# Kernel tuning notes

Measured on AMD Instinct MI355X. Metric: run time of the kernel, lower is better.

Reference implementation:

```python
import jax, jax.numpy as jnp
import numpy as np

EMBED_DIM = 1024
NUM_HEADS = 16
HEAD_DIM = EMBED_DIM // NUM_HEADS


def setup_inputs() -> dict:
    key = jax.random.key(0)
    ks = jax.random.split(key, 9)
    B, S, D = 4, 2048, EMBED_DIM
    s = 1.0 / np.sqrt(D)
    inp = {
        "x": jax.random.normal(ks[0], (B, S, D), dtype=jnp.float32),
        "Wq": jax.random.uniform(ks[1], (D, D), jnp.float32, -s, s),
        "bq": jax.random.uniform(ks[2], (D,), jnp.float32, -s, s),
        "Wk": jax.random.uniform(ks[3], (D, D), jnp.float32, -s, s),
        "bk": jax.random.uniform(ks[4], (D,), jnp.float32, -s, s),
        "Wv": jax.random.uniform(ks[5], (D, D), jnp.float32, -s, s),
        "bv": jax.random.uniform(ks[6], (D,), jnp.float32, -s, s),
        "Wo": jax.random.uniform(ks[7], (D, D), jnp.float32, -s, s),
        "bo": jax.random.uniform(ks[8], (D,), jnp.float32, -s, s),
    }
    return inp


def reference(x, Wq, bq, Wk, bk, Wv, bv, Wo, bo):
    B, S, D = x.shape
    H, Hd = NUM_HEADS, HEAD_DIM
    scale = 1.0 / jnp.sqrt(jnp.asarray(Hd, x.dtype))

    def split_heads(t):  # (B,S,D) -> (B,H,S,Hd)
        return t.reshape(B, S, H, Hd).transpose(0, 2, 1, 3)

    q = split_heads(x @ Wq + bq)
    k = split_heads(x @ Wk + bk)
    v = split_heads(x @ Wv + bv)

    scores = jnp.einsum("bhqd,bhkd->bhqk", q, k) * scale
    attn = jax.nn.softmax(scores, axis=-1)  # dropout is identity in eval mode
    out = jnp.einsum("bhqk,bhkd->bhqd", attn, v)
    out = out.transpose(0, 2, 1, 3).reshape(B, S, D)
    return out @ Wo + bo
```

## Files before the change

kernel.cpp:

```cpp
#include <hip/hip_runtime.h>
#include <cstdint>

typedef unsigned short u16;
typedef uint32_t u32;
typedef float f32x4 __attribute__((ext_vector_type(4)));
typedef short s16x8 __attribute__((ext_vector_type(8)));
typedef u16 u16x4 __attribute__((ext_vector_type(4)));
typedef u32 u32x2 __attribute__((ext_vector_type(2)));
typedef u32 u32x4 __attribute__((ext_vector_type(4)));

__device__ __forceinline__ u16 f2bf(float f) {
  u32 u = __builtin_bit_cast(u32, f);
  u += 0x7FFFu + ((u >> 16) & 1u);
  return (u16)(u >> 16);
}

__device__ __forceinline__ u32 pack2bf_trunc(float lo, float hi) {
  return __builtin_amdgcn_perm(__builtin_bit_cast(u32, hi),
                               __builtin_bit_cast(u32, lo), 0x07060302u);
}

template <typename T>
__device__ __forceinline__ T ldv(const void* p) {
  T v;
  __builtin_memcpy(&v, __builtin_assume_aligned(p, 16), sizeof(T));
  return v;
}

__device__ __forceinline__ void gload_lds16(const void* g, void* l) {
  __builtin_amdgcn_global_load_lds((const __attribute__((address_space(1))) void*)g,
                                   (__attribute__((address_space(3))) void*)l, 16, 0, 0);
}

__global__ __launch_bounds__(256) void cvt_x_k(const float* __restrict__ in,
                                               u16* __restrict__ out) {
  const int i = (blockIdx.x * 256 + threadIdx.x) * 4;
  float4 v = *(const float4*)(in + i);
  u16x4 o;
  o.x = f2bf(v.x); o.y = f2bf(v.y); o.z = f2bf(v.z); o.w = f2bf(v.w);
  *(u16x4*)(out + i) = o;
}

__global__ __launch_bounds__(256) void prep_w_k(const float* __restrict__ Wq,
                                                const float* __restrict__ Wk,
                                                const float* __restrict__ Wv,
                                                const float* __restrict__ Wo,
                                                u16* __restrict__ out) {
  __shared__ u16 t[64][72];
  const float* W = (blockIdx.z == 0) ? Wq : (blockIdx.z == 1) ? Wk
                  : (blockIdx.z == 2) ? Wv : Wo;
  u16* O = out + (size_t)blockIdx.z * 1024 * 1024;
  const int n0 = blockIdx.x * 64, k0 = blockIdx.y * 64;
  const int tid = threadIdx.x;
#pragma unroll
  for (int i = 0; i < 16; ++i) {
    int e = i * 256 + tid;
    int r = e >> 6, c = e & 63;
    t[r][c] = f2bf(W[(size_t)(k0 + r) * 1024 + n0 + c]);
  }
  __syncthreads();
#pragma unroll
  for (int i = 0; i < 16; ++i) {
    int e = i * 256 + tid;
    int rr = e >> 6, cc = e & 63;
    O[(size_t)(n0 + rr) * 1024 + k0 + cc] = t[cc][rr];
  }
}

__global__ __launch_bounds__(512, 2) void gemm_qkv_k(const u16* __restrict__ A,
                                                     const u16* __restrict__ Wt,
                                                     const float* __restrict__ bq,
                                                     const float* __restrict__ bk,
                                                     const float* __restrict__ bv,
                                                     u16* __restrict__ Qh,
                                                     u16* __restrict__ Kh,
                                                     u16* __restrict__ Vt,
                                                     float qscale) {
  constexpr int K = 1024;
  __shared__ __attribute__((aligned(16))) u16 As[3][256][64];
  __shared__ __attribute__((aligned(16))) u16 Bs[3][128][64];
  const int tid = threadIdx.x;
  const int l = tid & 63, w = tid >> 6;
  const int lr = l & 15, lg = l >> 4;
  const int m0 = blockIdx.x * 256;
  const int ng = blockIdx.y * 128;
  const int seg = ng >> 10;
  const int n0 = ng & 1023;
  const u16* Bt = Wt + ((size_t)seg << 20);
  const int wr = (w >> 1) * 64, wc = (w & 1) * 64;
  const int rT = tid >> 3;
  const int cSw = (((tid & 7) ^ (rT & 7)) << 3);

  f32x4 acc[4][4] = {};

#define GSTAGE(buf, kt)                                                         \
  do {                                                                          \
    _Pragma("unroll")                                                           \
    for (int i = 0; i < 4; ++i)                                                 \
      gload_lds16(A + (size_t)(m0 + i * 64 + rT) * K + (kt) + cSw,              \
                  &As[buf][i * 64][0] + (size_t)w * 512);                       \
    _Pragma("unroll")                                                           \
    for (int i = 0; i < 2; ++i)                                                 \
      gload_lds16(Bt + (size_t)(n0 + i * 64 + rT) * K + (kt) + cSw,             \
                  &Bs[buf][i * 64][0] + (size_t)w * 512);                       \
  } while (0)

  GSTAGE(0, 0);
  GSTAGE(1, 64);
  asm volatile("s_waitcnt vmcnt(6)" ::: "memory");
  __builtin_amdgcn_s_barrier();

  int bcur = 0, bst = 2;
  for (int t = 0; t < 16; ++t) {
    if (t < 14) {
      GSTAGE(bst, (t + 2) * 64);
      asm volatile("s_waitcnt vmcnt(12)" ::: "memory");
    } else if (t == 14) {
      asm volatile("s_waitcnt vmcnt(6)" ::: "memory");
    } else {
      asm volatile("s_waitcnt vmcnt(0)" ::: "memory");
    }
    __builtin_amdgcn_s_barrier();
#pragma unroll
    for (int kk = 0; kk < 2; ++kk) {
      s16x8 a[4], b[4];
#pragma unroll
      for (int mi = 0; mi < 4; ++mi)
        a[mi] = ldv<s16x8>(&As[bcur][wr + mi * 16 + lr][((kk * 4 + lg) ^ (lr & 7)) << 3]);
#pragma unroll
      for (int ni = 0; ni < 4; ++ni)
        b[ni] = ldv<s16x8>(&Bs[bcur][wc + ni * 16 + lr][((kk * 4 + lg) ^ (lr & 7)) << 3]);
#pragma unroll
      for (int mi = 0; mi < 4; ++mi)
#pragma unroll
        for (int ni = 0; ni < 4; ++ni)
          acc[mi][ni] = __builtin_amdgcn_mfma_f32_16x16x32_bf16(a[mi], b[ni], acc[mi][ni], 0, 0, 0);
    }
    __builtin_amdgcn_s_barrier();
    bcur = (bcur == 2) ? 0 : bcur + 1;
    bst = (bst == 2) ? 0 : bst + 1;
  }
#undef GSTAGE

  const float* bias = (seg == 0) ? bq : (seg == 1) ? bk : bv;
  const float scale = (seg == 0) ? qscale : 1.0f;
  u16* outp = (seg == 0) ? Qh : (seg == 1) ? Kh : Vt;

  u16* Cb = &As[0][0][0];
  const int bb = m0 >> 11;
  const int sbase = m0 & 2047;

#pragma unroll
  for (int p = 0; p < 2; ++p) {
    __syncthreads();
    if ((wc >> 6) == p) {
#pragma unroll
      for (int ni = 0; ni < 4; ++ni) {
        const int c = ni * 16 + lr;
        const float bvv = bias[n0 + p * 64 + c];
#pragma unroll
        for (int mi = 0; mi < 4; ++mi) {
#pragma unroll
          for (int r = 0; r < 4; ++r) {
            const int row = wr + mi * 16 + lg * 4 + r;
            Cb[row * 64 + ((((c >> 3) ^ (row & 7)) << 3) | (c & 7))] =
                f2bf((acc[mi][ni][r] + bvv) * scale);
          }
        }
      }
    }
    __syncthreads();
    const int h = (n0 + p * 64) >> 6;
    if (seg <= 1) {
      const int row = tid >> 1;
      const int s = sbase + row;
#pragma unroll
      for (int j = 0; j < 4; ++j) {
        const int c = (tid & 1) * 32 + j * 8;
        s16x8 v = ldv<s16x8>(&Cb[row * 64 + (((c >> 3) ^ (row & 7)) << 3)]);
        const int chunk = (seg == 0) ? (c >> 3) : (((c >> 3) ^ (s & 7)) & 7);
        *(s16x8*)(outp + ((size_t)((bb << 4) + h) * 2048 + s) * 64 + (chunk << 3)) = v;
      }
    } else {
      const int hd = tid & 63;
#pragma unroll
      for (int j = 0; j < 4; ++j) {
        const int s0 = (tid >> 6) * 32 + j * 8;
        u16 vals[8];
#pragma unroll
        for (int i = 0; i < 8; ++i) {
          const int row = s0 + i;
          vals[i] = Cb[row * 64 + ((((hd >> 3) ^ (row & 7)) << 3) | (hd & 7))];
        }
        const int sl = sbase + s0;
        const int swz = (((sl >> 3) & 7) ^ (hd & 7)) & 7;
        *(s16x8*)(outp + ((size_t)((bb << 4) + h) * 64 + hd) * 2048 +
                  ((sl & ~63) | (swz << 3))) = *(s16x8*)vals;
      }
    }
  }
}

__global__ __launch_bounds__(512, 2) void gemm_o_k(const u16* __restrict__ A,
                                                   const u16* __restrict__ Bt,
                                                   const float* __restrict__ bias,
                                                   float* __restrict__ outp) {
  constexpr int K = 1024;
  __shared__ __attribute__((aligned(16))) u16 As[3][256][64];
  __shared__ __attribute__((aligned(16))) u16 Bs[3][128][64];
  const int tid = threadIdx.x;
  const int l = tid & 63, w = tid >> 6;
  const int lr = l & 15, lg = l >> 4;
  const int m0 = blockIdx.x * 256, n0 = blockIdx.y * 128;
  const int wr = (w >> 1) * 64, wc = (w & 1) * 64;
  const int rT = tid >> 3;
  const int cSw = (((tid & 7) ^ (rT & 7)) << 3);

  f32x4 acc[4][4] = {};

#define GSTAGE(buf, kt)                                                         \
  do {                                                                          \
    _Pragma("unroll")                                                           \
    for (int i = 0; i < 4; ++i)                                                 \
      gload_lds16(A + (size_t)(m0 + i * 64 + rT) * K + (kt) + cSw,              \
                  &As[buf][i * 64][0] + (size_t)w * 512);                       \
    _Pragma("unroll")                                                           \
    for (int i = 0; i < 2; ++i)                                                 \
      gload_lds16(Bt + (size_t)(n0 + i * 64 + rT) * K + (kt) + cSw,             \
                  &Bs[buf][i * 64][0] + (size_t)w * 512);                       \
  } while (0)

  GSTAGE(0, 0);
  GSTAGE(1, 64);
  asm volatile("s_waitcnt vmcnt(6)" ::: "memory");
  __builtin_amdgcn_s_barrier();

  int bcur = 0, bst = 2;
  for (int t = 0; t < 16; ++t) {
    if (t < 14) {
      GSTAGE(bst, (t + 2) * 64);
      asm volatile("s_waitcnt vmcnt(12)" ::: "memory");
    } else if (t == 14) {
      asm volatile("s_waitcnt vmcnt(6)" ::: "memory");
    } else {
      asm volatile("s_waitcnt vmcnt(0)" ::: "memory");
    }
    __builtin_amdgcn_s_barrier();
#pragma unroll
    for (int kk = 0; kk < 2; ++kk) {
      s16x8 a[4], b[4];
#pragma unroll
      for (int mi = 0; mi < 4; ++mi)
        a[mi] = ldv<s16x8>(&As[bcur][wr + mi * 16 + lr][((kk * 4 + lg) ^ (lr & 7)) << 3]);
#pragma unroll
      for (int ni = 0; ni < 4; ++ni)
        b[ni] = ldv<s16x8>(&Bs[bcur][wc + ni * 16 + lr][((kk * 4 + lg) ^ (lr & 7)) << 3]);
#pragma unroll
      for (int mi = 0; mi < 4; ++mi)
#pragma unroll
        for (int ni = 0; ni < 4; ++ni)
          acc[mi][ni] = __builtin_amdgcn_mfma_f32_16x16x32_bf16(a[mi], b[ni], acc[mi][ni], 0, 0, 0);
    }
    __builtin_amdgcn_s_barrier();
    bcur = (bcur == 2) ? 0 : bcur + 1;
    bst = (bst == 2) ? 0 : bst + 1;
  }
#undef GSTAGE

#pragma unroll
  for (int ni = 0; ni < 4; ++ni) {
    const int col = n0 + wc + ni * 16 + lr;
    const float bv = bias[col];
#pragma unroll
    for (int mi = 0; mi < 4; ++mi)
#pragma unroll
      for (int r = 0; r < 4; ++r) {
        const int rowm = m0 + wr + mi * 16 + lg * 4 + r;
        outp[(size_t)rowm * 1024 + col] = acc[mi][ni][r] + bv;
      }
  }
}

__global__ __launch_bounds__(256, 2) void attn_k(const u16* __restrict__ Qh,
                                                 const u16* __restrict__ Kg,
                                                 const u16* __restrict__ Vg,
                                                 u16* __restrict__ Oattn) {
  __shared__ __attribute__((aligned(16))) u16 Kbuf[2][4096];
  __shared__ __attribute__((aligned(16))) u16 Vbuf[2][4096];
  __shared__ __attribute__((aligned(16))) u16 P_lds[4][16][64];
  const int tid = threadIdx.x, l = tid & 63, w = tid >> 6;
  const int lr = l & 15, lg = l >> 4;
  const int bh = blockIdx.y;
  const int q0 = blockIdx.x * 256 + w * 64;
  const u16* Q = Qh + (size_t)bh * (2048 * 64);
  const u16* K = Kg + (size_t)bh * (2048 * 64);
  const u16* V = Vg + (size_t)bh * (64 * 2048);

  s16x8 qf[4][2];
#pragma unroll
  for (int f = 0; f < 4; ++f)
#pragma unroll
    for (int kk = 0; kk < 2; ++kk)
      qf[f][kk] = ldv<s16x8>(Q + (size_t)(q0 + f * 16 + lr) * 64 + kk * 32 + lg * 8);

  const u32 one2 = 0x3F803F80u;
  const s16x8 onesv = __builtin_bit_cast(s16x8, (u32x4){one2, one2, one2, one2});

  f32x4 acc[4][4] = {};
  f32x4 lsum[4] = {};

#define STAGE(buf, kv0)                                                                 \
  do {                                                                                  \
    gload_lds16(K + (size_t)(kv0) * 64 + (size_t)tid * 8, &Kbuf[buf][w * 512]);         \
    gload_lds16(K + (size_t)(kv0) * 64 + 2048 + (size_t)tid * 8,                        \
                &Kbuf[buf][2048 + w * 512]);                                            \
    gload_lds16(V + (size_t)(tid >> 3) * 2048 + (kv0) + (tid & 7) * 8,                  \
                &Vbuf[buf][w * 512]);                                                   \
    gload_lds16(V + (size_t)((tid >> 3) + 32) * 2048 + (kv0) + (tid & 7) * 8,           \
                &Vbuf[buf][2048 + w * 512]);                                            \
  } while (0)

  STAGE(0, 0);

  for (int t = 0; t < 32; ++t) {
    const int cur = t & 1;
    if (t < 31) {
      STAGE(cur ^ 1, (t + 1) * 64);
      asm volatile("s_waitcnt vmcnt(4)" ::: "memory");
    } else {
      asm volatile("s_waitcnt vmcnt(0)" ::: "memory");
    }
    __builtin_amdgcn_s_barrier();

    s16x8 pf[4][2];
#pragma unroll
    for (int kvc = 0; kvc < 2; ++kvc) {
      f32x4 s2[4][2] = {};
      __builtin_amdgcn_s_setprio(1);
#pragma unroll
      for (int t2 = 0; t2 < 2; ++t2) {
        const int tt = kvc * 2 + t2;
        s16x8 k0 = ldv<s16x8>(&Kbuf[cur][(tt * 16 + lr) * 64 + ((lg ^ (lr & 7)) << 3)]);
        s16x8 k1 = ldv<s16x8>(&Kbuf[cur][(tt * 16 + lr) * 64 + (((4 + lg) ^ (lr & 7)) << 3)]);
#pragma unroll
        for (int f = 0; f < 4; ++f) {
          s2[f][t2] = __builtin_amdgcn_mfma_f32_16x16x32_bf16(k0, qf[f][0], s2[f][t2], 0, 0, 0);
          s2[f][t2] = __builtin_amdgcn_mfma_f32_16x16x32_bf16(k1, qf[f][1], s2[f][t2], 0, 0, 0);
        }
      }
      __builtin_amdgcn_s_setprio(0);

#pragma unroll
      for (int f = 0; f < 4; ++f) {
#pragma unroll
        for (int t2 = 0; t2 < 2; ++t2)
#pragma unroll
          for (int r = 0; r < 4; ++r)
            s2[f][t2][r] = __builtin_amdgcn_exp2f(s2[f][t2][r]);
#pragma unroll
        for (int t2 = 0; t2 < 2; ++t2) {
          const int tt = kvc * 2 + t2;
          u32x2 pw;
          pw.x = pack2bf_trunc(s2[f][t2][0], s2[f][t2][1]);
          pw.y = pack2bf_trunc(s2[f][t2][2], s2[f][t2][3]);
          const int off = (((tt * 2 + (lg >> 1)) ^ (lr & 7)) << 3) + ((lg & 1) << 2);
          *(u32x2*)&P_lds[w][lr][off] = pw;
        }
        pf[f][kvc] = ldv<s16x8>(&P_lds[w][lr][((kvc * 4 + lg) ^ (lr & 7)) << 3]);
        lsum[f] = __builtin_amdgcn_mfma_f32_16x16x32_bf16(pf[f][kvc], onesv, lsum[f], 0, 0, 0);
      }
    }

    __builtin_amdgcn_s_setprio(1);
#pragma unroll
    for (int dt = 0; dt < 4; ++dt) {
      s16x8 v0 = ldv<s16x8>(&Vbuf[cur][(dt * 16 + lr) * 64 + ((lg ^ (lr & 7)) << 3)]);
      s16x8 v1 = ldv<s16x8>(&Vbuf[cur][(dt * 16 + lr) * 64 + (((4 + lg) ^ (lr & 7)) << 3)]);
#pragma unroll
      for (int f = 0; f < 4; ++f) {
        acc[f][dt] = __builtin_amdgcn_mfma_f32_16x16x32_bf16(pf[f][0], v0, acc[f][dt], 0, 0, 0);
        acc[f][dt] = __builtin_amdgcn_mfma_f32_16x16x32_bf16(pf[f][1], v1, acc[f][dt], 0, 0, 0);
      }
    }
    __builtin_amdgcn_s_setprio(0);
    __builtin_amdgcn_s_barrier();
  }
#undef STAGE

  const int b = bh >> 4, h = bh & 15;
#pragma unroll
  for (int f = 0; f < 4; ++f) {
    float li[4];
#pragma unroll
    for (int r = 0; r < 4; ++r) li[r] = __builtin_amdgcn_rcpf(lsum[f][r]);
#pragma unroll
    for (int dt = 0; dt < 4; ++dt)
#pragma unroll
      for (int r = 0; r < 4; ++r) {
        const int q = q0 + f * 16 + lg * 4 + r;
        Oattn[(size_t)((b << 11) + q) * 1024 + (h << 6) + dt * 16 + lr] =
            f2bf(acc[f][dt][r] * li[r]);
      }
  }
}

extern "C" void kernel_launch(void* const* d_in, const int* in_sizes, int n_in,
                              void* d_out, int out_size, void* d_ws, size_t ws_size,
                              hipStream_t stream) {
  const float* x  = (const float*)d_in[0];
  const float* Wq = (const float*)d_in[1];
  const float* bq = (const float*)d_in[2];
  const float* Wk = (const float*)d_in[3];
  const float* bk = (const float*)d_in[4];
  const float* Wv = (const float*)d_in[5];
  const float* bv = (const float*)d_in[6];
  const float* Wo = (const float*)d_in[7];
  const float* bo = (const float*)d_in[8];

  char* ws = (char*)d_ws;
  const size_t MB = 1u << 20;
  u16* xb = (u16*)(ws);
  u16* wt = (u16*)(ws + 16 * MB);
  u16* Qh = (u16*)(ws + 24 * MB);
  u16* Kh = (u16*)(ws + 40 * MB);
  u16* Vt = (u16*)(ws + 56 * MB);
  u16* attn = xb;

  const float qscale = 0.125f * 1.44269504088896f;

  cvt_x_k<<<dim3(8192), dim3(256), 0, stream>>>(x, xb);
  prep_w_k<<<dim3(16, 16, 4), dim3(256), 0, stream>>>(Wq, Wk, Wv, Wo, wt);
  gemm_qkv_k<<<dim3(32, 24), dim3(512), 0, stream>>>(xb, wt, bq, bk, bv, Qh, Kh, Vt, qscale);
  attn_k<<<dim3(8, 64), dim3(256), 0, stream>>>(Qh, Kh, Vt, attn);
  gemm_o_k<<<dim3(32, 8), dim3(512), 0, stream>>>(attn, wt + 3 * 1048576, bo, (float*)d_out);
}
```

Baseline: 201.7 us.

## Merge QKV and output GEMMs into one templated 256x256-tile kernel

Replaces the 256x128-tile GEMMs with one templated 256x256-tile kernel. It has 8 waves each computing 128x64, double buffering instead of triple, and occupancy 1. Larger tiles raise arithmetic intensity and reuse of the loaded A and B tiles. In exchange the output GEMM launches only 128 blocks, under half the CUs, and the QKV GEMM 384, so CU utilization and latency hiding may drop.

Result: slower. 227.3 us (+12.7%).

```diff
diff --git a/kernel.cpp b/kernel.cpp
--- a/kernel.cpp
+++ b/kernel.cpp
@@ -67,31 +67,34 @@
   }
 }
 
-__global__ __launch_bounds__(512, 2) void gemm_qkv_k(const u16* __restrict__ A,
-                                                     const u16* __restrict__ Wt,
-                                                     const float* __restrict__ bq,
-                                                     const float* __restrict__ bk,
-                                                     const float* __restrict__ bv,
-                                                     u16* __restrict__ Qh,
-                                                     u16* __restrict__ Kh,
-                                                     u16* __restrict__ Vt,
-                                                     float qscale) {
+template <int OMODE>
+__global__ __launch_bounds__(512, 1) void gemm256_k(const u16* __restrict__ A,
+                                                    const u16* __restrict__ Wt,
+                                                    const float* __restrict__ bq,
+                                                    const float* __restrict__ bk,
+                                                    const float* __restrict__ bv,
+                                                    u16* __restrict__ Qh,
+                                                    u16* __restrict__ Kh,
+                                                    u16* __restrict__ Vt,
+                                                    float* __restrict__ Oo,
+                                                    float qscale) {
   constexpr int K = 1024;
-  __shared__ __attribute__((aligned(16))) u16 As[3][256][64];
-  __shared__ __attribute__((aligned(16))) u16 Bs[3][128][64];
+  __shared__ __attribute__((aligned(16))) u16 As[2][256][64];
+  __shared__ __attribute__((aligned(16))) u16 Bs[2][256][64];
   const int tid = threadIdx.x;
   const int l = tid & 63, w = tid >> 6;
   const int lr = l & 15, lg = l >> 4;
+  const int wm = w >> 2, wn = w & 3;
   const int m0 = blockIdx.x * 256;
-  const int ng = blockIdx.y * 128;
-  const int seg = ng >> 10;
-  const int n0 = ng & 1023;
+  int seg, n0;
+  if constexpr (OMODE == 0) { seg = blockIdx.y >> 2; n0 = (blockIdx.y & 3) * 256; }
+  else { seg = 3; n0 = blockIdx.y * 256; }
   const u16* Bt = Wt + ((size_t)seg << 20);
-  const int wr = (w >> 1) * 64, wc = (w & 1) * 64;
   const int rT = tid >> 3;
   const int cSw = (((tid & 7) ^ (rT & 7)) << 3);
-
-  f32x4 acc[4][4] = {};
+  const int xk = lr & 7;
+
+  f32x4 acc[8][4] = {};
 
 #define GSTAGE(buf, kt)                                                         \
   do {                                                                          \
@@ -100,184 +103,111 @@
       gload_lds16(A + (size_t)(m0 + i * 64 + rT) * K + (kt) + cSw,              \
                   &As[buf][i * 64][0] + (size_t)w * 512);                       \
     _Pragma("unroll")                                                           \
-    for (int i = 0; i < 2; ++i)                                                 \
+    for (int i = 0; i < 4; ++i)                                                 \
       gload_lds16(Bt + (size_t)(n0 + i * 64 + rT) * K + (kt) + cSw,             \
                   &Bs[buf][i * 64][0] + (size_t)w * 512);                       \
   } while (0)
 
   GSTAGE(0, 0);
-  GSTAGE(1, 64);
-  asm volatile("s_waitcnt vmcnt(6)" ::: "memory");
+  asm volatile("s_waitcnt vmcnt(0)" ::: "memory");
   __builtin_amdgcn_s_barrier();
 
-  int bcur = 0, bst = 2;
   for (int t = 0; t < 16; ++t) {
-    if (t < 14) {
-      GSTAGE(bst, (t + 2) * 64);
-      asm volatile("s_waitcnt vmcnt(12)" ::: "memory");
-    } else if (t == 14) {
-      asm volatile("s_waitcnt vmcnt(6)" ::: "memory");
+    const int cur = t & 1;
+    if (t < 15) {
+      GSTAGE(cur ^ 1, (t + 1) * 64);
+      asm volatile("s_waitcnt vmcnt(8)" ::: "memory");
     } else {
       asm volatile("s_waitcnt vmcnt(0)" ::: "memory");
     }
     __builtin_amdgcn_s_barrier();
 #pragma unroll
     for (int kk = 0; kk < 2; ++kk) {
-      s16x8 a[4], b[4];
-#pragma unroll
-      for (int mi = 0; mi < 4; ++mi)
-        a[mi] = ldv<s16x8>(&As[bcur][wr + mi * 16 + lr][((kk * 4 + lg) ^ (lr & 7)) << 3]);
+      s16x8 b[4];
 #pragma unroll
       for (int ni = 0; ni < 4; ++ni)
-        b[ni] = ldv<s16x8>(&Bs[bcur][wc + ni * 16 + lr][((kk * 4 + lg) ^ (lr & 7)) << 3]);
-#pragma unroll
-      for (int mi = 0; mi < 4; ++mi)
+        b[ni] = ldv<s16x8>(&Bs[cur][wn * 64 + ni * 16 + lr][((kk * 4 + lg) ^ xk) << 3]);
+#pragma unroll
+      for (int mi = 0; mi < 8; ++mi) {
+        s16x8 a = ldv<s16x8>(&As[cur][wm * 128 + mi * 16 + lr][((kk * 4 + lg) ^ xk) << 3]);
 #pragma unroll
         for (int ni = 0; ni < 4; ++ni)
-          acc[mi][ni] = __builtin_amdgcn_mfma_f32_16x16x32_bf16(a[mi], b[ni], acc[mi][ni], 0, 0, 0);
+          acc[mi][ni] = __builtin_amdgcn_mfma_f32_16x16x32_bf16(a, b[ni], acc[mi][ni], 0, 0, 0);
+      }
     }
     __builtin_amdgcn_s_barrier();
-    bcur = (bcur == 2) ? 0 : bcur + 1;
-    bst = (bst == 2) ? 0 : bst + 1;
   }
 #undef GSTAGE
 
-  const float* bias = (seg == 0) ? bq : (seg == 1) ? bk : bv;
-  const float scale = (seg == 0) ? qscale : 1.0f;
-  u16* outp = (seg == 0) ? Qh : (seg == 1) ? Kh : Vt;
-
-  u16* Cb = &As[0][0][0];
-  const int bb = m0 >> 11;
-  const int sbase = m0 & 2047;
-
-#pragma unroll
-  for (int p = 0; p < 2; ++p) {
-    __syncthreads();
-    if ((wc >> 6) == p) {
-#pragma unroll
-      for (int ni = 0; ni < 4; ++ni) {
-        const int c = ni * 16 + lr;
-        const float bvv = bias[n0 + p * 64 + c];
-#pragma unroll
-        for (int mi = 0; mi < 4; ++mi) {
-#pragma unroll
-          for (int r = 0; r < 4; ++r) {
-            const int row = wr + mi * 16 + lg * 4 + r;
-            Cb[row * 64 + ((((c >> 3) ^ (row & 7)) << 3) | (c & 7))] =
-                f2bf((acc[mi][ni][r] + bvv) * scale);
+  if constexpr (OMODE == 1) {
+#pragma unroll
+    for (int ni = 0; ni < 4; ++ni) {
+      const int col = n0 + wn * 64 + ni * 16 + lr;
+      const float bvv = bq[col];
+#pragma unroll
+      for (int mi = 0; mi < 8; ++mi)
+#pragma unroll
+        for (int r = 0; r < 4; ++r) {
+          const int row = m0 + wm * 128 + mi * 16 + lg * 4 + r;
+          Oo[(size_t)row * 1024 + col] = acc[mi][ni][r] + bvv;
+        }
+    }
+    return;
+  } else {
+    const float* bias = (seg == 0) ? bq : (seg == 1) ? bk : bv;
+    const float scale = (seg == 0) ? qscale : 1.0f;
+    u16* outp = (seg == 0) ? Qh : (seg == 1) ? Kh : Vt;
+    u16* Cb = &As[0][0][0];
+    const int bb = m0 >> 11;
+    const int sbase = m0 & 2047;
+#pragma unroll
+    for (int p = 0; p < 4; ++p) {
+      __syncthreads();
+      if (wn == p) {
+#pragma unroll
+        for (int ni = 0; ni < 4; ++ni) {
+          const int c = ni * 16 + lr;
+          const float bvv = bias[n0 + p * 64 + c];
+#pragma unroll
+          for (int mi = 0; mi < 8; ++mi)
+#pragma unroll
+            for (int r = 0; r < 4; ++r) {
+              const int row = wm * 128 + mi * 16 + lg * 4 + r;
+              Cb[row * 64 + ((((c >> 3) ^ (row & 7)) << 3) | (c & 7))] =
+                  f2bf((acc[mi][ni][r] + bvv) * scale);
+            }
+        }
+      }
+      __syncthreads();
+      const int h = (n0 + p * 64) >> 6;
+      if (seg <= 1) {
+        const int row = tid >> 1;
+        const int s = sbase + row;
+#pragma unroll
+        for (int j = 0; j < 4; ++j) {
+          const int c = (tid & 1) * 32 + j * 8;
+          s16x8 v = ldv<s16x8>(&Cb[row * 64 + (((c >> 3) ^ (row & 7)) << 3)]);
+          const int chunk = (seg == 0) ? (c >> 3) : (((c >> 3) ^ (s & 7)) & 7);
+          *(s16x8*)(outp + ((size_t)((bb << 4) + h) * 2048 + s) * 64 + (chunk << 3)) = v;
+        }
+      } else {
+        const int hd = tid & 63;
+#pragma unroll
+        for (int j = 0; j < 4; ++j) {
+          const int s0 = (tid >> 6) * 32 + j * 8;
+          u16 vals[8];
+#pragma unroll
+          for (int i = 0; i < 8; ++i) {
+            const int row = s0 + i;
+            vals[i] = Cb[row * 64 + ((((hd >> 3) ^ (row & 7)) << 3) | (hd & 7))];
           }
-        }
-      }
-    }
-    __syncthreads();
-    const int h = (n0 + p * 64) >> 6;
-    if (seg <= 1) {
-      const int row = tid >> 1;
-      const int s = sbase + row;
-#pragma unroll
-      for (int j = 0; j < 4; ++j) {
-        const int c = (tid & 1) * 32 + j * 8;
-        s16x8 v = ldv<s16x8>(&Cb[row * 64 + (((c >> 3) ^ (row & 7)) << 3)]);
-        const int chunk = (seg == 0) ? (c >> 3) : (((c >> 3) ^ (s & 7)) & 7);
-        *(s16x8*)(outp + ((size_t)((bb << 4) + h) * 2048 + s) * 64 + (chunk << 3)) = v;
-      }
-    } else {
-      const int hd = tid & 63;
-#pragma unroll
-      for (int j = 0; j < 4; ++j) {
-        const int s0 = (tid >> 6) * 32 + j * 8;
-        u16 vals[8];
-#pragma unroll
-        for (int i = 0; i < 8; ++i) {
-          const int row = s0 + i;
-          vals[i] = Cb[row * 64 + ((((hd >> 3) ^ (row & 7)) << 3) | (hd & 7))];
-        }
-        const int sl = sbase + s0;
-        const int swz = (((sl >> 3) & 7) ^ (hd & 7)) & 7;
-        *(s16x8*)(outp + ((size_t)((bb << 4) + h) * 64 + hd) * 2048 +
-                  ((sl & ~63) | (swz << 3))) = *(s16x8*)vals;
-      }
-    }
-  }
-}
-
-__global__ __launch_bounds__(512, 2) void gemm_o_k(const u16* __restrict__ A,
-                                                   const u16* __restrict__ Bt,
-                                                   const float* __restrict__ bias,
-                                                   float* __restrict__ outp) {
-  constexpr int K = 1024;
-  __shared__ __attribute__((aligned(16))) u16 As[3][256][64];
-  __shared__ __attribute__((aligned(16))) u16 Bs[3][128][64];
-  const int tid = threadIdx.x;
-  const int l = tid & 63, w = tid >> 6;
-  const int lr = l & 15, lg = l >> 4;
-  const int m0 = blockIdx.x * 256, n0 = blockIdx.y * 128;
-  const int wr = (w >> 1) * 64, wc = (w & 1) * 64;
-  const int rT = tid >> 3;
-  const int cSw = (((tid & 7) ^ (rT & 7)) << 3);
-
-  f32x4 acc[4][4] = {};
-
-#define GSTAGE(buf, kt)                                                         \
-  do {                                                                          \
-    _Pragma("unroll")                                                           \
-    for (int i = 0; i < 4; ++i)                                                 \
-      gload_lds16(A + (size_t)(m0 + i * 64 + rT) * K + (kt) + cSw,              \
-                  &As[buf][i * 64][0] + (size_t)w * 512);                       \
-    _Pragma("unroll")                                                           \
-    for (int i = 0; i < 2; ++i)                                                 \
-      gload_lds16(Bt + (size_t)(n0 + i * 64 + rT) * K + (kt) + cSw,             \
-                  &Bs[buf][i * 64][0] + (size_t)w * 512);                       \
-  } while (0)
-
-  GSTAGE(0, 0);
-  GSTAGE(1, 64);
-  asm volatile("s_waitcnt vmcnt(6)" ::: "memory");
-  __builtin_amdgcn_s_barrier();
-
-  int bcur = 0, bst = 2;
-  for (int t = 0; t < 16; ++t) {
-    if (t < 14) {
-      GSTAGE(bst, (t + 2) * 64);
-      asm volatile("s_waitcnt vmcnt(12)" ::: "memory");
-    } else if (t == 14) {
-      asm volatile("s_waitcnt vmcnt(6)" ::: "memory");
-    } else {
-      asm volatile("s_waitcnt vmcnt(0)" ::: "memory");
-    }
-    __builtin_amdgcn_s_barrier();
-#pragma unroll
-    for (int kk = 0; kk < 2; ++kk) {
-      s16x8 a[4], b[4];
-#pragma unroll
-      for (int mi = 0; mi < 4; ++mi)
-        a[mi] = ldv<s16x8>(&As[bcur][wr + mi * 16 + lr][((kk * 4 + lg) ^ (lr & 7)) << 3]);
-#pragma unroll
-      for (int ni = 0; ni < 4; ++ni)
-        b[ni] = ldv<s16x8>(&Bs[bcur][wc + ni * 16 + lr][((kk * 4 + lg) ^ (lr & 7)) << 3]);
-#pragma unroll
-      for (int mi = 0; mi < 4; ++mi)
-#pragma unroll
-        for (int ni = 0; ni < 4; ++ni)
-          acc[mi][ni] = __builtin_amdgcn_mfma_f32_16x16x32_bf16(a[mi], b[ni], acc[mi][ni], 0, 0, 0);
-    }
-    __builtin_amdgcn_s_barrier();
-    bcur = (bcur == 2) ? 0 : bcur + 1;
-    bst = (bst == 2) ? 0 : bst + 1;
-  }
-#undef GSTAGE
-
-#pragma unroll
-  for (int ni = 0; ni < 4; ++ni) {
-    const int col = n0 + wc + ni * 16 + lr;
-    const float bv = bias[col];
-#pragma unroll
-    for (int mi = 0; mi < 4; ++mi)
-#pragma unroll
-      for (int r = 0; r < 4; ++r) {
-        const int rowm = m0 + wr + mi * 16 + lg * 4 + r;
-        outp[(size_t)rowm * 1024 + col] = acc[mi][ni][r] + bv;
-      }
+          const int sl = sbase + s0;
+          const int swz = (((sl >> 3) & 7) ^ (hd & 7)) & 7;
+          *(s16x8*)(outp + ((size_t)((bb << 4) + h) * 64 + hd) * 2048 +
+                    ((sl & ~63) | (swz << 3))) = *(s16x8*)vals;
+        }
+      }
+    }
   }
 }
 
@@ -430,7 +360,10 @@
 
   cvt_x_k<<<dim3(8192), dim3(256), 0, stream>>>(x, xb);
   prep_w_k<<<dim3(16, 16, 4), dim3(256), 0, stream>>>(Wq, Wk, Wv, Wo, wt);
-  gemm_qkv_k<<<dim3(32, 24), dim3(512), 0, stream>>>(xb, wt, bq, bk, bv, Qh, Kh, Vt, qscale);
+  gemm256_k<0><<<dim3(32, 12), dim3(512), 0, stream>>>(xb, wt, bq, bk, bv, Qh, Kh, Vt,
+                                                       nullptr, qscale);
   attn_k<<<dim3(8, 64), dim3(256), 0, stream>>>(Qh, Kh, Vt, attn);
-  gemm_o_k<<<dim3(32, 8), dim3(512), 0, stream>>>(attn, wt + 3 * 1048576, bo, (float*)d_out);
-}
+  gemm256_k<1><<<dim3(32, 4), dim3(512), 0, stream>>>(attn, wt, bo, nullptr, nullptr,
+                                                      nullptr, nullptr, nullptr,
+                                                      (float*)d_out, 1.0f);
+}
```

## Enlarge QKV GEMM tile to 256x384 and double attention block to 8 waves

Applied to the files above, without the earlier changes.

The QKV GEMM moves from a 256x128 tile with a triple-buffered pipeline to a 256x384 tile with double buffering. Each wave now holds an 8x6 MFMA accumulator tile, and the epilogue writes scalar bf16 directly to global memory instead of going through LDS and vector stores. The attention kernel now uses 512 threads with 8 waves sharing each K/V tile load, which halves the per-thread staging work. The intent is more operand reuse and fewer K/V loads, at the cost of higher register pressure, lower occupancy (launch bounds 1), a shallower prefetch pipeline, and uncoalesced scalar stores in the GEMM epilogue.

New measurement: 208.9 us. 3.6% more time.

```diff
diff --git a/kernel.cpp b/kernel.cpp
--- a/kernel.cpp
+++ b/kernel.cpp
@@ -67,7 +67,7 @@
   }
 }
 
-__global__ __launch_bounds__(512, 2) void gemm_qkv_k(const u16* __restrict__ A,
+__global__ __launch_bounds__(512, 1) void gemm_qkv_k(const u16* __restrict__ A,
                                                      const u16* __restrict__ Wt,
                                                      const float* __restrict__ bq,
                                                      const float* __restrict__ bk,
@@ -77,21 +77,19 @@
                                                      u16* __restrict__ Vt,
                                                      float qscale) {
   constexpr int K = 1024;
-  __shared__ __attribute__((aligned(16))) u16 As[3][256][64];
-  __shared__ __attribute__((aligned(16))) u16 Bs[3][128][64];
+  __shared__ __attribute__((aligned(16))) u16 As[2][256][64];
+  __shared__ __attribute__((aligned(16))) u16 Bs[2][384][64];
   const int tid = threadIdx.x;
   const int l = tid & 63, w = tid >> 6;
   const int lr = l & 15, lg = l >> 4;
+  const int wm = w >> 2, wn = w & 3;
   const int m0 = blockIdx.x * 256;
-  const int ng = blockIdx.y * 128;
-  const int seg = ng >> 10;
-  const int n0 = ng & 1023;
-  const u16* Bt = Wt + ((size_t)seg << 20);
-  const int wr = (w >> 1) * 64, wc = (w & 1) * 64;
+  const int by = blockIdx.y;
   const int rT = tid >> 3;
   const int cSw = (((tid & 7) ^ (rT & 7)) << 3);
-
-  f32x4 acc[4][4] = {};
+  const int xk = lr & 7;
+
+  f32x4 acc[8][6] = {};
 
 #define GSTAGE(buf, kt)                                                         \
   do {                                                                          \
@@ -100,102 +98,70 @@
       gload_lds16(A + (size_t)(m0 + i * 64 + rT) * K + (kt) + cSw,              \
                   &As[buf][i * 64][0] + (size_t)w * 512);                       \
     _Pragma("unroll")                                                           \
-    for (int i = 0; i < 2; ++i)                                                 \
-      gload_lds16(Bt + (size_t)(n0 + i * 64 + rT) * K + (kt) + cSw,             \
+    for (int i = 0; i < 6; ++i)                                                 \
+      gload_lds16(Wt + (size_t)(by * 384 + i * 64 + rT) * K + (kt) + cSw,       \
                   &Bs[buf][i * 64][0] + (size_t)w * 512);                       \
   } while (0)
 
   GSTAGE(0, 0);
-  GSTAGE(1, 64);
-  asm volatile("s_waitcnt vmcnt(6)" ::: "memory");
+  asm volatile("s_waitcnt vmcnt(0)" ::: "memory");
   __builtin_amdgcn_s_barrier();
 
-  int bcur = 0, bst = 2;
   for (int t = 0; t < 16; ++t) {
-    if (t < 14) {
-      GSTAGE(bst, (t + 2) * 64);
-      asm volatile("s_waitcnt vmcnt(12)" ::: "memory");
-    } else if (t == 14) {
-      asm volatile("s_waitcnt vmcnt(6)" ::: "memory");
+    const int cur = t & 1;
+    if (t < 15) {
+      GSTAGE(cur ^ 1, (t + 1) * 64);
+      asm volatile("s_waitcnt vmcnt(10)" ::: "memory");
     } else {
       asm volatile("s_waitcnt vmcnt(0)" ::: "memory");
     }
     __builtin_amdgcn_s_barrier();
 #pragma unroll
     for (int kk = 0; kk < 2; ++kk) {
-      s16x8 a[4], b[4];
-#pragma unroll
-      for (int mi = 0; mi < 4; ++mi)
-        a[mi] = ldv<s16x8>(&As[bcur][wr + mi * 16 + lr][((kk * 4 + lg) ^ (lr & 7)) << 3]);
-#pragma unroll
-      for (int ni = 0; ni < 4; ++ni)
-        b[ni] = ldv<s16x8>(&Bs[bcur][wc + ni * 16 + lr][((kk * 4 + lg) ^ (lr & 7)) << 3]);
-#pragma unroll
-      for (int mi = 0; mi < 4; ++mi)
-#pragma unroll
-        for (int ni = 0; ni < 4; ++ni)
-          acc[mi][ni] = __builtin_amdgcn_mfma_f32_16x16x32_bf16(a[mi], b[ni], acc[mi][ni], 0, 0, 0);
-    }
-    __builtin_amdgcn_s_barrier();
-    bcur = (bcur == 2) ? 0 : bcur + 1;
-    bst = (bst == 2) ? 0 : bst + 1;
+      s16x8 b[6];
+#pragma unroll
+      for (int ni = 0; ni < 6; ++ni)
+        b[ni] = ldv<s16x8>(&Bs[cur][wn * 96 + ni * 16 + lr][((kk * 4 + lg) ^ xk) << 3]);
+#pragma unroll
+      for (int mi = 0; mi < 8; ++mi) {
+        s16x8 a = ldv<s16x8>(&As[cur][wm * 128 + mi * 16 + lr][((kk * 4 + lg) ^ xk) << 3]);
+#pragma unroll
+        for (int ni = 0; ni < 6; ++ni)
+          acc[mi][ni] = __builtin_amdgcn_mfma_f32_16x16x32_bf16(a, b[ni], acc[mi][ni], 0, 0, 0);
+      }
+    }
+    __builtin_amdgcn_s_barrier();
   }
 #undef GSTAGE
 
-  const float* bias = (seg == 0) ? bq : (seg == 1) ? bk : bv;
-  const float scale = (seg == 0) ? qscale : 1.0f;
-  u16* outp = (seg == 0) ? Qh : (seg == 1) ? Kh : Vt;
-
-  u16* Cb = &As[0][0][0];
-  const int bb = m0 >> 11;
-  const int sbase = m0 & 2047;
-
-#pragma unroll
-  for (int p = 0; p < 2; ++p) {
-    __syncthreads();
-    if ((wc >> 6) == p) {
-#pragma unroll
-      for (int ni = 0; ni < 4; ++ni) {
-        const int c = ni * 16 + lr;
-        const float bvv = bias[n0 + p * 64 + c];
-#pragma unroll
-        for (int mi = 0; mi < 4; ++mi) {
-#pragma unroll
-          for (int r = 0; r < 4; ++r) {
-            const int row = wr + mi * 16 + lg * 4 + r;
-            Cb[row * 64 + ((((c >> 3) ^ (row & 7)) << 3) | (c & 7))] =
-                f2bf((acc[mi][ni][r] + bvv) * scale);
-          }
+  const int gcbase = by * 384 + wn * 96;
+#pragma unroll
+  for (int ni = 0; ni < 6; ++ni) {
+    const int gc0 = gcbase + ni * 16;
+    const int seg = gc0 >> 10;
+    const int col = (gc0 & 1023) + lr;
+    const float* bias = (seg == 0) ? bq : (seg == 1) ? bk : bv;
+    u16* outp = (seg == 0) ? Qh : (seg == 1) ? Kh : Vt;
+    const float scale = (seg == 0) ? qscale : 1.0f;
+    const float bvv = bias[col];
+    const int h = col >> 6, hd = col & 63;
+#pragma unroll
+    for (int mi = 0; mi < 8; ++mi) {
+#pragma unroll
+      for (int r = 0; r < 4; ++r) {
+        const int row = m0 + wm * 128 + mi * 16 + lg * 4 + r;
+        const float v = (acc[mi][ni][r] + bvv) * scale;
+        const int bb = row >> 11, s = row & 2047;
+        const u16 o = f2bf(v);
+        if (seg == 0) {
+          outp[((size_t)((bb << 4) + h) * 2048 + s) * 64 + hd] = o;
+        } else if (seg == 1) {
+          const int hd_swz = ((((hd >> 3) ^ (s & 7)) & 7) << 3) | (hd & 7);
+          outp[((size_t)((bb << 4) + h) * 2048 + s) * 64 + hd_swz] = o;
+        } else {
+          const int s_swz = (s & ~63) | (((((s >> 3) & 7) ^ (hd & 7)) & 7) << 3) | (s & 7);
+          outp[((size_t)((bb << 4) + h) * 64 + hd) * 2048 + s_swz] = o;
         }
-      }
-    }
-    __syncthreads();
-    const int h = (n0 + p * 64) >> 6;
-    if (seg <= 1) {
-      const int row = tid >> 1;
-      const int s = sbase + row;
-#pragma unroll
-      for (int j = 0; j < 4; ++j) {
-        const int c = (tid & 1) * 32 + j * 8;
-        s16x8 v = ldv<s16x8>(&Cb[row * 64 + (((c >> 3) ^ (row & 7)) << 3)]);
-        const int chunk = (seg == 0) ? (c >> 3) : (((c >> 3) ^ (s & 7)) & 7);
-        *(s16x8*)(outp + ((size_t)((bb << 4) + h) * 2048 + s) * 64 + (chunk << 3)) = v;
-      }
-    } else {
-      const int hd = tid & 63;
-#pragma unroll
-      for (int j = 0; j < 4; ++j) {
-        const int s0 = (tid >> 6) * 32 + j * 8;
-        u16 vals[8];
-#pragma unroll
-        for (int i = 0; i < 8; ++i) {
-          const int row = s0 + i;
-          vals[i] = Cb[row * 64 + ((((hd >> 3) ^ (row & 7)) << 3) | (hd & 7))];
-        }
-        const int sl = sbase + s0;
-        const int swz = (((sl >> 3) & 7) ^ (hd & 7)) & 7;
-        *(s16x8*)(outp + ((size_t)((bb << 4) + h) * 64 + hd) * 2048 +
-                  ((sl & ~63) | (swz << 3))) = *(s16x8*)vals;
       }
     }
   }
@@ -281,17 +247,17 @@
   }
 }
 
-__global__ __launch_bounds__(256, 2) void attn_k(const u16* __restrict__ Qh,
+__global__ __launch_bounds__(512, 1) void attn_k(const u16* __restrict__ Qh,
                                                  const u16* __restrict__ Kg,
                                                  const u16* __restrict__ Vg,
                                                  u16* __restrict__ Oattn) {
   __shared__ __attribute__((aligned(16))) u16 Kbuf[2][4096];
   __shared__ __attribute__((aligned(16))) u16 Vbuf[2][4096];
-  __shared__ __attribute__((aligned(16))) u16 P_lds[4][16][64];
+  __shared__ __attribute__((aligned(16))) u16 P_lds[8][16][64];
   const int tid = threadIdx.x, l = tid & 63, w = tid >> 6;
   const int lr = l & 15, lg = l >> 4;
   const int bh = blockIdx.y;
-  const int q0 = blockIdx.x * 256 + w * 64;
+  const int q0 = blockIdx.x * 512 + w * 64;
   const u16* Q = Qh + (size_t)bh * (2048 * 64);
   const u16* K = Kg + (size_t)bh * (2048 * 64);
   const u16* V = Vg + (size_t)bh * (64 * 2048);
@@ -312,12 +278,8 @@
 #define STAGE(buf, kv0)                                                                 \
   do {                                                                                  \
     gload_lds16(K + (size_t)(kv0) * 64 + (size_t)tid * 8, &Kbuf[buf][w * 512]);         \
-    gload_lds16(K + (size_t)(kv0) * 64 + 2048 + (size_t)tid * 8,                        \
-                &Kbuf[buf][2048 + w * 512]);                                            \
     gload_lds16(V + (size_t)(tid >> 3) * 2048 + (kv0) + (tid & 7) * 8,                  \
                 &Vbuf[buf][w * 512]);                                                   \
-    gload_lds16(V + (size_t)((tid >> 3) + 32) * 2048 + (kv0) + (tid & 7) * 8,           \
-                &Vbuf[buf][2048 + w * 512]);                                            \
   } while (0)
 
   STAGE(0, 0);
@@ -326,7 +288,7 @@
     const int cur = t & 1;
     if (t < 31) {
       STAGE(cur ^ 1, (t + 1) * 64);
-      asm volatile("s_waitcnt vmcnt(4)" ::: "memory");
+      asm volatile("s_waitcnt vmcnt(2)" ::: "memory");
     } else {
       asm volatile("s_waitcnt vmcnt(0)" ::: "memory");
     }
@@ -430,7 +392,7 @@
 
   cvt_x_k<<<dim3(8192), dim3(256), 0, stream>>>(x, xb);
   prep_w_k<<<dim3(16, 16, 4), dim3(256), 0, stream>>>(Wq, Wk, Wv, Wo, wt);
-  gemm_qkv_k<<<dim3(32, 24), dim3(512), 0, stream>>>(xb, wt, bq, bk, bv, Qh, Kh, Vt, qscale);
-  attn_k<<<dim3(8, 64), dim3(256), 0, stream>>>(Qh, Kh, Vt, attn);
+  gemm_qkv_k<<<dim3(32, 8), dim3(512), 0, stream>>>(xb, wt, bq, bk, bv, Qh, Kh, Vt, qscale);
+  attn_k<<<dim3(4, 64), dim3(512), 0, stream>>>(Qh, Kh, Vt, attn);
   gemm_o_k<<<dim3(32, 8), dim3(512), 0, stream>>>(attn, wt + 3 * 1048576, bo, (float*)d_out);
 }
```
